# Performance work log

Hardware: AMD Instinct MI355X
Metric: run time of the kernel (lower is better)

The kernel has to match this reference:

```python
import jax, jax.numpy as jnp
import numpy as np

B, Q, G = 32, 16384, 128   # batch, num queries, (padded) num GT per image
K = 32                      # first top-k (nearest candidates per GT)
N = 9                       # second top-k (highest-IoU matches per GT)


def box_cxcywh_to_xyxy(b):
    cx, cy, w, h = jnp.split(b, 4, axis=-1)
    return jnp.concatenate([cx - 0.5 * w, cy - 0.5 * h,
                            cx + 0.5 * w, cy + 0.5 * h], axis=-1)


def box_iou(a, b):
    # a, b: broadcastable [..., 4] in xyxy
    lt = jnp.maximum(a[..., :2], b[..., :2])
    rb = jnp.minimum(a[..., 2:], b[..., 2:])
    wh = jnp.clip(rb - lt, 0.0)
    inter = wh[..., 0] * wh[..., 1]
    area_a = (a[..., 2] - a[..., 0]) * (a[..., 3] - a[..., 1])
    area_b = (b[..., 2] - b[..., 0]) * (b[..., 3] - b[..., 1])
    return inter / (area_a + area_b - inter)


def _assign(gt, pred):
    # gt: [G,4] cxcywh, pred: [Q,4] cxcywh
    # euclidean cdist in cxcywh space: [G, Q]
    d = jnp.sqrt(jnp.sum((gt[:, None, :] - pred[None, :, :]) ** 2, axis=-1))
    # k nearest predictions per GT (smallest distance)
    _, kidx = jax.lax.top_k(-d, K)            # [G, K]
    k_boxes = pred[kidx]                       # [G, K, 4]
    iou = box_iou(box_cxcywh_to_xyxy(gt)[:, None, :],
                  box_cxcywh_to_xyxy(k_boxes))           # [G, K]
    vals, ns = jax.lax.top_k(iou, N)           # [G, N] highest IoU among the K
    pred_idx = jnp.take_along_axis(kidx, ns, axis=1)      # [G, N] global pred ids
    gt_idx = jnp.broadcast_to(jnp.arange(gt.shape[0])[:, None], ns.shape)
    return pred_idx.reshape(-1), gt_idx.reshape(-1)


def setup_inputs() -> dict:
    key = jax.random.key(0)
    k1, k2 = jax.random.split(key)
    pred_boxes = jax.random.uniform(k1, (B, Q, 4), dtype=jnp.float32)
    gt_boxes = jax.random.uniform(k2, (B, G, 4), dtype=jnp.float32)
    return {"pred_boxes": pred_boxes, "gt_boxes": gt_boxes}


def reference(pred_boxes, gt_boxes):
    # per-image assignment, vectorized over the batch
    pred_idx, gt_idx = jax.vmap(_assign)(gt_boxes, pred_boxes)
    # pred_idx, gt_idx: [B, G*N] int32 (analog of the list of (i, j) index tensors)
    return pred_idx, gt_idx
```

## Files before the change

kernel.cpp:

```cpp
#include <hip/hip_runtime.h>

#define BB 32
#define QQ 16384
#define GG 128
#define KK 32
#define NN 9
#define TT 8
#define TH 1024
#define RR (QQ / TH)
#define NW (TH / 64)
#define CAP 192
#define ACAP 96
#define UF 4

typedef unsigned long long u64;
typedef unsigned int u32;

#define INFF __uint_as_float(0x7F800000u)

__device__ __forceinline__ u64 pack_asc(float key, u32 idx) {
  return (((u64)__float_as_uint(key)) << 32) | (u64)idx;
}

__device__ __forceinline__ float dist2_ref(const float4 g, const float4 p) {
#pragma clang fp contract(off)
  float dx = g.x - p.x;
  float dy = g.y - p.y;
  float dz = g.z - p.z;
  float dw = g.w - p.w;
  float s = dx * dx + dy * dy;
  s = s + dz * dz;
  s = s + dw * dw;
  return s;
}

__device__ __forceinline__ float iou_ref(const float4 g, const float4 p) {
#pragma clang fp contract(off)
  float gx1 = g.x - 0.5f * g.z, gy1 = g.y - 0.5f * g.w;
  float gx2 = g.x + 0.5f * g.z, gy2 = g.y + 0.5f * g.w;
  float px1 = p.x - 0.5f * p.z, py1 = p.y - 0.5f * p.w;
  float px2 = p.x + 0.5f * p.z, py2 = p.y + 0.5f * p.w;
  float ltx = fmaxf(gx1, px1), lty = fmaxf(gy1, py1);
  float rbx = fminf(gx2, px2), rby = fminf(gy2, py2);
  float wx = fmaxf(rbx - ltx, 0.0f), wy = fmaxf(rby - lty, 0.0f);
  float inter = wx * wy;
  float aa = (gx2 - gx1) * (gy2 - gy1);
  float ab = (px2 - px1) * (py2 - py1);
  return inter / ((aa + ab) - inter);
}

__device__ __forceinline__ u64 bitonic64(u64 v, int lane) {
#pragma unroll
  for (int k = 2; k <= 64; k <<= 1) {
#pragma unroll
    for (int j = k >> 1; j > 0; j >>= 1) {
      u64 o = __shfl_xor(v, j, 64);
      bool up = ((lane & k) == 0);
      bool lower = ((lane & j) == 0);
      v = (lower == up) ? (v < o ? v : o) : (v > o ? v : o);
    }
  }
  return v;
}

__device__ __forceinline__ float bitonic64f(float v, int lane) {
#pragma unroll
  for (int k = 2; k <= 64; k <<= 1) {
#pragma unroll
    for (int j = k >> 1; j > 0; j >>= 1) {
      float o = __shfl_xor(v, j, 64);
      bool up = ((lane & k) == 0);
      bool lower = ((lane & j) == 0);
      v = (lower == up) ? fminf(v, o) : fmaxf(v, o);
    }
  }
  return v;
}

__global__ __launch_bounds__(TH, 8) void atss_kernel(
    const float4* __restrict__ pred, const float4* __restrict__ gtb,
    int* __restrict__ out) {
  __shared__ float smin[TT][TH];
  __shared__ float ckey[TT][CAP];
  __shared__ unsigned short cidx[TT][CAP];
  __shared__ unsigned short sact[TT][ACAP];
  __shared__ int kidx[TT][KK];
  __shared__ int nC[TT];
  __shared__ int nAct[TT];

  const int t = threadIdx.x;
  const int f = blockIdx.x;
  const int b = (f & 7) * 4 + (f >> 7);
  const int g0 = ((f >> 3) & 15) * TT;

  if (t < TT) {
    nC[t] = 0;
    nAct[t] = 0;
  }

  float4 G[TT];
#pragma unroll
  for (int gg = 0; gg < TT; ++gg) G[gg] = gtb[b * GG + g0 + gg];

  const float4* pb = pred + (size_t)b * QQ;

  float mn[TT];
#pragma unroll
  for (int gg = 0; gg < TT; ++gg) mn[gg] = INFF;

  float4 P[UF];
#pragma unroll
  for (int u = 0; u < UF; ++u) P[u] = pb[t + u * TH];
#pragma unroll
  for (int j = 0; j < RR; j += UF) {
    float4 C[UF];
#pragma unroll
    for (int u = 0; u < UF; ++u) C[u] = P[u];
    if (j + UF < RR) {
#pragma unroll
      for (int u = 0; u < UF; ++u) P[u] = pb[t + (j + UF + u) * TH];
    }
#pragma unroll
    for (int u = 0; u < UF; ++u) {
      float4 p = C[u];
      float pp = fmaf(p.x, p.x, fmaf(p.y, p.y, fmaf(p.z, p.z, p.w * p.w)));
#pragma unroll
      for (int gg = 0; gg < TT; ++gg) {
        float dot = fmaf(G[gg].x, p.x,
                    fmaf(G[gg].y, p.y,
                    fmaf(G[gg].z, p.z, G[gg].w * p.w)));
        mn[gg] = fminf(mn[gg], fmaf(-2.0f, dot, pp));
      }
    }
  }
#pragma unroll
  for (int gg = 0; gg < TT; ++gg) smin[gg][t] = mn[gg];

  __syncthreads();

  const int w = t >> 6;
  const int lane = t & 63;
  if (w >= TT) return;

  const float4 gt = gtb[b * GG + g0 + w];

  float V[NW];
#pragma unroll
  for (int k = 0; k < NW; ++k) V[k] = smin[w][lane + 64 * k];

  float m1 = INFF, m2 = INFF;
#pragma unroll
  for (int k = 0; k < NW; ++k) {
    float v = V[k];
    float nm1 = fminf(m1, v);
    m2 = fminf(m2, fmaxf(m1, v));
    m1 = nm1;
  }

  float A = bitonic64f(m1, lane);
  float Bs = bitonic64f(m2, lane);
  float Br = __shfl(Bs, 63 - lane, 64);
  float m = fminf(A, Br);
#pragma unroll
  for (int j = 32; j > 0; j >>= 1) {
    float o = __shfl_xor(m, j, 64);
    m = ((lane & j) == 0) ? fminf(m, o) : fmaxf(m, o);
  }
  float Us = __shfl(m, 31, 64);
  float gg2 = fmaf(gt.x, gt.x,
              fmaf(gt.y, gt.y, fmaf(gt.z, gt.z, gt.w * gt.w)));
  const float sUs = Us + fabsf(Us) * 2e-5f + 4e-6f;
  const float T = fmaxf(Us + gg2, 0.0f) * 1.00002f + 4e-6f;

#pragma unroll
  for (int k = 0; k < NW; ++k) {
    if (V[k] <= sUs) {
      int pos = atomicAdd(&nAct[w], 1);
      if (pos < ACAP) sact[w][pos] = (unsigned short)(lane + 64 * k);
    }
  }
  int na = nAct[w];

  if (na <= ACAP) {
    for (int it = lane; it < na; it += 64) {
      int r = sact[w][it];
      for (int j = 0; j < RR; ++j) {
        int i = r + j * TH;
        float d2 = dist2_ref(gt, pb[i]);
        if (d2 <= T) {
          int pos = atomicAdd(&nC[w], 1);
          if (pos < CAP) {
            ckey[w][pos] = d2;
            cidx[w][pos] = (unsigned short)i;
          }
        }
      }
    }
  } else {
    for (int r = lane; r < TH; r += 64) {
      for (int j = 0; j < RR; ++j) {
        int i = r + j * TH;
        float d2 = dist2_ref(gt, pb[i]);
        if (d2 <= T) {
          int pos = atomicAdd(&nC[w], 1);
          if (pos < CAP) {
            ckey[w][pos] = d2;
            cidx[w][pos] = (unsigned short)i;
          }
        }
      }
    }
  }
  int n = nC[w];

  if (n > CAP) {
    if (lane == 0) {
      u64 best[KK];
      for (int l = 0; l < KK; ++l) best[l] = ~0ull;
      for (int i = 0; i < QQ; ++i) {
        float d = sqrtf(dist2_ref(gt, pb[i]));
        u64 pk = pack_asc(d, (u32)i);
        if (pk < best[KK - 1]) {
          int pos = KK - 1;
          while (pos > 0 && best[pos - 1] > pk) {
            best[pos] = best[pos - 1];
            --pos;
          }
          best[pos] = pk;
        }
      }
      for (int l = 0; l < KK; ++l) kidx[w][l] = (int)(best[l] & 0xFFFFFFFFull);
    }
  } else if (n <= 64) {
    u64 v = (lane < n) ? pack_asc(sqrtf(ckey[w][lane]), (u32)cidx[w][lane])
                       : ~0ull;
    u64 s = bitonic64(v, lane);
    if (lane < KK) kidx[w][lane] = (int)(s & 0xFFFFFFFFull);
  } else {
    volatile float* vk = ckey[w];
    for (int sel = 0; sel < KK; ++sel) {
      u64 lm = ~0ull;
      int ls = -1;
      for (int s = lane; s < n; s += 64) {
        float d = sqrtf(vk[s]);
        u64 pk = pack_asc(d, (u32)cidx[w][s]);
        if (pk < lm) {
          lm = pk;
          ls = s;
        }
      }
      u64 ww = lm;
#pragma unroll
      for (int j = 32; j > 0; j >>= 1) {
        u64 o = __shfl_xor(ww, j, 64);
        ww = o < ww ? o : ww;
      }
      if (lm == ww && ls >= 0) {
        vk[ls] = INFF;
        kidx[w][sel] = (int)(ww & 0xFFFFFFFFull);
      }
    }
  }

  {
    u64 v = ~0ull;
    if (lane < KK) {
      float iou = iou_ref(gt, pb[kidx[w][lane]]);
      v = (((u64)(~__float_as_uint(iou))) << 32) | (u64)lane;
    }
    u64 s = bitonic64(v, lane);
    if (lane < NN) {
      int pos = (int)(s & 0xFFFFFFFFull);
      int base = (b * GG + g0 + w) * NN + lane;
      out[base] = kidx[w][pos];
      out[BB * GG * NN + base] = g0 + w;
    }
  }
}

extern "C" void kernel_launch(void* const* d_in, const int* in_sizes, int n_in,
                              void* d_out, int out_size, void* d_ws, size_t ws_size,
                              hipStream_t stream) {
  (void)in_sizes;
  (void)n_in;
  (void)out_size;
  (void)d_ws;
  (void)ws_size;
  const float4* pred = (const float4*)d_in[0];
  const float4* gt = (const float4*)d_in[1];
  int* out = (int*)d_out;
  atss_kernel<<<(GG / TT) * BB, TH, 0, stream>>>(pred, gt, out);
}
```

Baseline: 78.27 us.

## Process 16 GTs per block with one wave each and flatten candidate rescan

Doubles the GTs handled per block from 8 to 16, so each predicted box loaded during the min-distance pass is reused across more GTs and all 16 waves take part in the per-GT selection phase. The distance accumulation is folded into four FMAs using pre-doubled prediction coordinates. The candidate rescan is flattened across (row, repeat) pairs so all lanes get balanced work, and the final IoU sort uses a 32-wide bitonic network. The cost is more registers and shared memory per block (launch bounds drop to 4) and half as many blocks, which lowers occupancy and parallelism across CUs.

```diff
diff --git a/kernel.cpp b/kernel.cpp
--- a/kernel.cpp
+++ b/kernel.cpp
@@ -5,7 +5,7 @@
 #define GG 128
 #define KK 32
 #define NN 9
-#define TT 8
+#define TT 16
 #define TH 1024
 #define RR (QQ / TH)
 #define NW (TH / 64)
@@ -63,6 +63,20 @@
   return v;
 }
 
+__device__ __forceinline__ u64 bitonic32(u64 v, int lane) {
+#pragma unroll
+  for (int k = 2; k <= 32; k <<= 1) {
+#pragma unroll
+    for (int j = k >> 1; j > 0; j >>= 1) {
+      u64 o = __shfl_xor(v, j, 64);
+      bool up = ((lane & k) == 0);
+      bool lower = ((lane & j) == 0);
+      v = (lower == up) ? (v < o ? v : o) : (v > o ? v : o);
+    }
+  }
+  return v;
+}
+
 __device__ __forceinline__ float bitonic64f(float v, int lane) {
 #pragma unroll
   for (int k = 2; k <= 64; k <<= 1) {
@@ -77,7 +91,7 @@
   return v;
 }
 
-__global__ __launch_bounds__(TH, 8) void atss_kernel(
+__global__ __launch_bounds__(TH, 4) void atss_kernel(
     const float4* __restrict__ pred, const float4* __restrict__ gtb,
     int* __restrict__ out) {
   __shared__ float smin[TT][TH];
@@ -90,8 +104,8 @@
 
   const int t = threadIdx.x;
   const int f = blockIdx.x;
-  const int b = (f & 7) * 4 + (f >> 7);
-  const int g0 = ((f >> 3) & 15) * TT;
+  const int b = (f & 7) * 4 + (f >> 6);
+  const int g0 = ((f >> 3) & 7) * TT;
 
   if (t < TT) {
     nC[t] = 0;
@@ -124,12 +138,14 @@
     for (int u = 0; u < UF; ++u) {
       float4 p = C[u];
       float pp = fmaf(p.x, p.x, fmaf(p.y, p.y, fmaf(p.z, p.z, p.w * p.w)));
+      float qx = p.x + p.x, qy = p.y + p.y, qz = p.z + p.z, qw = p.w + p.w;
 #pragma unroll
       for (int gg = 0; gg < TT; ++gg) {
-        float dot = fmaf(G[gg].x, p.x,
-                    fmaf(G[gg].y, p.y,
-                    fmaf(G[gg].z, p.z, G[gg].w * p.w)));
-        mn[gg] = fminf(mn[gg], fmaf(-2.0f, dot, pp));
+        float acc = fmaf(-G[gg].x, qx, pp);
+        acc = fmaf(-G[gg].y, qy, acc);
+        acc = fmaf(-G[gg].z, qz, acc);
+        acc = fmaf(-G[gg].w, qw, acc);
+        mn[gg] = fminf(mn[gg], acc);
       }
     }
   }
@@ -140,7 +156,6 @@
 
   const int w = t >> 6;
   const int lane = t & 63;
-  if (w >= TT) return;
 
   const float4 gt = gtb[b * GG + g0 + w];
 
@@ -182,17 +197,16 @@
   int na = nAct[w];
 
   if (na <= ACAP) {
-    for (int it = lane; it < na; it += 64) {
-      int r = sact[w][it];
-      for (int j = 0; j < RR; ++j) {
-        int i = r + j * TH;
-        float d2 = dist2_ref(gt, pb[i]);
-        if (d2 <= T) {
-          int pos = atomicAdd(&nC[w], 1);
-          if (pos < CAP) {
-            ckey[w][pos] = d2;
-            cidx[w][pos] = (unsigned short)i;
-          }
+    int total = na * RR;
+    for (int it = lane; it < total; it += 64) {
+      int r = sact[w][it >> 4];
+      int i = r + (it & 15) * TH;
+      float d2 = dist2_ref(gt, pb[i]);
+      if (d2 <= T) {
+        int pos = atomicAdd(&nC[w], 1);
+        if (pos < CAP) {
+          ckey[w][pos] = d2;
+          cidx[w][pos] = (unsigned short)i;
         }
       }
     }
@@ -268,7 +282,7 @@
       float iou = iou_ref(gt, pb[kidx[w][lane]]);
       v = (((u64)(~__float_as_uint(iou))) << 32) | (u64)lane;
     }
-    u64 s = bitonic64(v, lane);
+    u64 s = bitonic32(v, lane);
     if (lane < NN) {
       int pos = (int)(s & 0xFFFFFFFFull);
       int base = (b * GG + g0 + w) * NN + lane;
```

New measurement: 80.24 us. +2.5%, slower.
